# Kernel optimization log

Measured on AMD Instinct MI355X. Metric: run time of the kernel, lower is better.

The kernel has to match this reference:

```python
import jax, jax.numpy as jnp
import numpy as np

DEGREE = 7

def setup_inputs() -> dict:
    key = jax.random.key(0)
    k1, k2 = jax.random.split(key)
    input_dims, output_dims = 1024, 1024
    x = jax.random.normal(k1, (8192, input_dims), dtype=jnp.float32)
    std = 1.0 / (input_dims * (DEGREE + 1))
    lucas_coeffs = std * jax.random.normal(k2, (input_dims, output_dims, DEGREE + 1), dtype=jnp.float32)
    return {"x": x, "lucas_coeffs": lucas_coeffs}

def reference(x, lucas_coeffs):
    input_dims = lucas_coeffs.shape[0]
    x = x.reshape(-1, input_dims)
    x = jnp.tanh(x)
    # Lucas polynomial recurrence: L0=2, L1=x, L_i = x*L_{i-1} + L_{i-2}
    basis = [jnp.full_like(x, 2.0)]
    if DEGREE > 0:
        basis.append(x)
    for i in range(2, DEGREE + 1):
        basis.append(x * basis[-1] + basis[-2])
    lucas = jnp.stack(basis, axis=-1)  # [b, i, d]
    y = jnp.einsum('bid,iod->bo', lucas, lucas_coeffs)
    return y
```

## Files before the change

### kernel.cpp

```cpp
#include <hip/hip_runtime.h>
#include <hip/hip_bf16.h>


typedef __attribute__((ext_vector_type(8)))  short  short8;
typedef __attribute__((ext_vector_type(8)))  unsigned short ushort8;
typedef __attribute__((ext_vector_type(4)))  float  float4v;
typedef __attribute__((ext_vector_type(16))) float  float16v;
typedef __attribute__((ext_vector_type(4)))  unsigned int uint4v;

#define M_DIM 8192
#define I_DIM 1024
#define O_DIM 1024
#define K_DIM 8192
#define BM 256
#define BN 128
#define BK 64
#define KSPLIT 2
#define KHALF (K_DIM / KSPLIT)
#define NSTEP (KHALF / BK)

__device__ __forceinline__ unsigned short f2bf(float f) {
    unsigned int u = __float_as_uint(f);
    u += 0x7FFFu + ((u >> 16) & 1u);
    return (unsigned short)(u >> 16);
}

__global__ __launch_bounds__(256) void prep_kernel(const float* __restrict__ x,
                                                   const float* __restrict__ c,
                                                   unsigned short* __restrict__ T,
                                                   unsigned short* __restrict__ Bt,
                                                   float* __restrict__ outz) {
    int bid = blockIdx.x;
    const int zPart = (M_DIM * O_DIM) / (4 * 256);
    const int tPart = (M_DIM * I_DIM) / (8 * 256);
    if (bid < zPart) {
        int idx = (bid * 256 + threadIdx.x) * 4;
        const float4v z = {0.f, 0.f, 0.f, 0.f};
        *(float4v*)(outz + idx) = z;
    } else if (bid < zPart + tPart) {
        int idx = ((bid - zPart) * 256 + threadIdx.x) * 8;
        float4v v0 = *(const float4v*)(x + idx);
        float4v v1 = *(const float4v*)(x + idx + 4);
        unsigned short t[8];
        t[0] = f2bf(tanhf(v0[0])); t[1] = f2bf(tanhf(v0[1]));
        t[2] = f2bf(tanhf(v0[2])); t[3] = f2bf(tanhf(v0[3]));
        t[4] = f2bf(tanhf(v1[0])); t[5] = f2bf(tanhf(v1[1]));
        t[6] = f2bf(tanhf(v1[2])); t[7] = f2bf(tanhf(v1[3]));
        ushort8 o;
        #pragma unroll
        for (int p = 0; p < 4; ++p) { o[p] = t[2 * p]; o[4 + p] = t[2 * p + 1]; }
        *(ushort8*)(T + idx) = o;
    } else {
        int idx = (bid - zPart - tPart) * 256 + threadIdx.x;
        int i = idx >> 10;
        int o = idx & 1023;
        const float* src = c + (size_t)i * 8192 + o * 8;
        float4v lo = *(const float4v*)(src);
        float4v hi = *(const float4v*)(src + 4);
        ushort8 v;
        v[0] = f2bf(lo[0]); v[1] = f2bf(lo[1]); v[2] = f2bf(lo[2]); v[3] = f2bf(lo[3]);
        v[4] = f2bf(hi[0]); v[5] = f2bf(hi[1]); v[6] = f2bf(hi[2]); v[7] = f2bf(hi[3]);
        *(ushort8*)(Bt + (size_t)o * K_DIM + i * 8) = v;
    }
}

__device__ __forceinline__ short8 lucas_frag(unsigned int tb) {
    const float t = __uint_as_float(tb << 16);
    const float L2v = fmaf(t, t, 2.0f);
    const float L3v = fmaf(t, L2v, t);
    const float L4v = fmaf(t, L3v, L2v);
    const float L5v = fmaf(t, L4v, L3v);
    const float L6v = fmaf(t, L5v, L4v);
    const float L7v = fmaf(t, L6v, L5v);
    union { uint4v u; short8 s; } r;
#if __has_builtin(__builtin_amdgcn_cvt_pk_bf16_f32)
    {
        auto p0 = __builtin_amdgcn_cvt_pk_bf16_f32(2.0f, t);
        auto p1 = __builtin_amdgcn_cvt_pk_bf16_f32(L2v, L3v);
        auto p2 = __builtin_amdgcn_cvt_pk_bf16_f32(L4v, L5v);
        auto p3 = __builtin_amdgcn_cvt_pk_bf16_f32(L6v, L7v);
        __builtin_memcpy(&r.u[0], &p0, 4);
        __builtin_memcpy(&r.u[1], &p1, 4);
        __builtin_memcpy(&r.u[2], &p2, 4);
        __builtin_memcpy(&r.u[3], &p3, 4);
    }
#else
    {
        r.u[0] = 0x4000u | (tb << 16);
        r.u[1] = __builtin_amdgcn_perm(__float_as_uint(L3v), __float_as_uint(L2v), 0x07060302);
        r.u[2] = __builtin_amdgcn_perm(__float_as_uint(L5v), __float_as_uint(L4v), 0x07060302);
        r.u[3] = __builtin_amdgcn_perm(__float_as_uint(L7v), __float_as_uint(L6v), 0x07060302);
    }
#endif
    return r.s;
}

__global__ __launch_bounds__(256, 2) void gemm_kernel(const unsigned short* __restrict__ T,
                                                      const unsigned short* __restrict__ Bt,
                                                      float* __restrict__ out) {
    __shared__ unsigned short Bs[2][BN * BK];
    __shared__ unsigned short Ts[2][BM * 8];

    const int tid  = threadIdx.x;
    const int lane = tid & 63;
    const int wave = tid >> 6;
    const int n0 = blockIdx.x * BN;
    const int m0 = blockIdx.y * BM;
    const int k0 = blockIdx.z * KHALF;

    const int l32 = lane & 31;
    const int h   = lane >> 5;
    const int wml = wave * 64;

    const int srow   = lane >> 3;
    const int il     = lane & 7;
    const int gchunk = il ^ srow;

    float16v acc[2][4];
    #pragma unroll
    for (int a = 0; a < 2; ++a)
        #pragma unroll
        for (int b = 0; b < 4; ++b)
            #pragma unroll
            for (int e = 0; e < 16; ++e) acc[a][b][e] = 0.f;

    auto stage = [&](int buf, int kt) {
        #pragma unroll
        for (int r = 0; r < 4; ++r) {
            const int rowb = r * 32 + wave * 8;
            const unsigned short* gB = Bt + (size_t)(n0 + rowb + srow) * K_DIM + kt + gchunk * 8;
            __builtin_amdgcn_global_load_lds(
                (const __attribute__((address_space(1))) unsigned int*)gB,
                (__attribute__((address_space(3))) unsigned int*)&Bs[buf][rowb * BK], 16, 0, 0);
        }
        const unsigned short* gT = T + (size_t)(m0 + wml + lane) * I_DIM + kt / 8;
        __builtin_amdgcn_global_load_lds(
            (const __attribute__((address_space(1))) unsigned int*)gT,
            (__attribute__((address_space(3))) unsigned int*)&Ts[buf][wml * 8], 16, 0, 0);
    };

    stage(0, k0);
    __syncthreads();

    int cur = 0;
    for (int s = 0; s < NSTEP; ++s) {
        const int nxt = cur ^ 1;
        if (s + 1 < NSTEP) stage(nxt, k0 + (s + 1) * BK);

        unsigned long long tw[2];
        #pragma unroll
        for (int tt = 0; tt < 2; ++tt)
            tw[tt] = *(const unsigned long long*)&Ts[cur][(wml + tt * 32 + l32) * 8 + h * 4];

        #pragma unroll
        for (int kk = 0; kk < 4; ++kk) {
            short8 bfr[4];
            #pragma unroll
            for (int tn = 0; tn < 4; ++tn) {
                const int brow = tn * 32 + l32;
                bfr[tn] = *(const short8*)&Bs[cur][brow * BK + (((kk * 2 + h) ^ (brow & 7)) * 8)];
            }
            #pragma unroll
            for (int tt = 0; tt < 2; ++tt) {
                const short8 af = lucas_frag((unsigned int)((tw[tt] >> (16 * kk)) & 0xffffu));
                #pragma unroll
                for (int tn = 0; tn < 4; ++tn)
                    acc[tt][tn] = __builtin_amdgcn_mfma_f32_32x32x16_bf16(
                        af, bfr[tn], acc[tt][tn], 0, 0, 0);
            }
        }

        __syncthreads();
        cur = nxt;
    }

    #pragma unroll
    for (int tt = 0; tt < 2; ++tt) {
        #pragma unroll
        for (int tn = 0; tn < 4; ++tn) {
            const int col = n0 + tn * 32 + l32;
            #pragma unroll
            for (int reg = 0; reg < 16; ++reg) {
                const int row = m0 + wml + tt * 32 + (reg & 3) + 8 * (reg >> 2) + 4 * h;
                atomicAdd(&out[(size_t)row * O_DIM + col], acc[tt][tn][reg]);
            }
        }
    }
}

__global__ __launch_bounds__(256) void naive_kernel(const float* __restrict__ x,
                                                    const float* __restrict__ c,
                                                    float* __restrict__ out) {
    int idx = blockIdx.x * 256 + threadIdx.x;
    int b = idx >> 10;
    int o = idx & 1023;
    const float* xb = x + (size_t)b * I_DIM;
    float acc = 0.f;
    for (int i = 0; i < I_DIM; ++i) {
        float t = tanhf(xb[i]);
        float L[8];
        L[0] = 2.0f; L[1] = t;
        #pragma unroll
        for (int d = 2; d < 8; ++d) L[d] = t * L[d - 1] + L[d - 2];
        const float* cc = c + (size_t)i * 8192 + o * 8;
        #pragma unroll
        for (int d = 0; d < 8; ++d) acc += L[d] * cc[d];
    }
    out[idx] = acc;
}

extern "C" void kernel_launch(void* const* d_in, const int* in_sizes, int n_in,
                              void* d_out, int out_size, void* d_ws, size_t ws_size,
                              hipStream_t stream) {
    const float* x      = (const float*)d_in[0];
    const float* coeffs = (const float*)d_in[1];
    float* out = (float*)d_out;

    const size_t btBytes = (size_t)O_DIM * K_DIM * sizeof(unsigned short);
    const size_t tBytes  = (size_t)M_DIM * I_DIM * sizeof(unsigned short);

    if (ws_size >= btBytes + tBytes) {
        unsigned short* Bt = (unsigned short*)d_ws;
        unsigned short* T  = (unsigned short*)((char*)d_ws + btBytes);

        const int zBlocks = (M_DIM * O_DIM) / (4 * 256);
        const int tBlocks = (M_DIM * I_DIM) / (8 * 256);
        const int bBlocks = (I_DIM * O_DIM) / 256;
        prep_kernel<<<zBlocks + tBlocks + bBlocks, 256, 0, stream>>>(x, coeffs, T, Bt, out);

        dim3 grid(O_DIM / BN, M_DIM / BM, KSPLIT);
        gemm_kernel<<<grid, 256, 0, stream>>>(T, Bt, out);
    } else {
        naive_kernel<<<(M_DIM * O_DIM) / 256, 256, 0, stream>>>(x, coeffs, out);
    }
}
```

Baseline: 259.9 us.

## Shrink GEMM tile to 128x128 with 2x2 waves and LDS-transpose coefficient prep

The GEMM block tile is reduced from 256x128 to 128x128, with the four waves arranged 2x2 (64x64 each) instead of stacked along M. Accumulators per thread are halved and the occupancy hint is raised to 4 blocks per SM, giving twice as many blocks and more latency hiding. The trade is less B-tile reuse per block and more global traffic. Separately, the coefficient prep kernel now stages a 64x32 tile in shared memory, so both its reads of the fp32 coefficients and its writes of the transposed bf16 array are coalesced.

```diff
diff --git a/kernel.cpp b/kernel.cpp
--- a/kernel.cpp
+++ b/kernel.cpp
@@ -3,6 +3,7 @@
 
 
 typedef __attribute__((ext_vector_type(8)))  short  short8;
+typedef __attribute__((ext_vector_type(4)))  unsigned short ushort4v;
 typedef __attribute__((ext_vector_type(8)))  unsigned short ushort8;
 typedef __attribute__((ext_vector_type(4)))  float  float4v;
 typedef __attribute__((ext_vector_type(16))) float  float16v;
@@ -12,7 +13,7 @@
 #define I_DIM 1024
 #define O_DIM 1024
 #define K_DIM 8192
-#define BM 256
+#define BM 128
 #define BN 128
 #define BK 64
 #define KSPLIT 2
@@ -30,15 +31,16 @@
                                                    unsigned short* __restrict__ T,
                                                    unsigned short* __restrict__ Bt,
                                                    float* __restrict__ outz) {
-    int bid = blockIdx.x;
     const int zPart = (M_DIM * O_DIM) / (4 * 256);
     const int tPart = (M_DIM * I_DIM) / (8 * 256);
+    int bid = blockIdx.x;
+    int tid = threadIdx.x;
     if (bid < zPart) {
-        int idx = (bid * 256 + threadIdx.x) * 4;
+        int idx = (bid * 256 + tid) * 4;
         const float4v z = {0.f, 0.f, 0.f, 0.f};
         *(float4v*)(outz + idx) = z;
     } else if (bid < zPart + tPart) {
-        int idx = ((bid - zPart) * 256 + threadIdx.x) * 8;
+        int idx = ((bid - zPart) * 256 + tid) * 8;
         float4v v0 = *(const float4v*)(x + idx);
         float4v v1 = *(const float4v*)(x + idx + 4);
         unsigned short t[8];
@@ -51,16 +53,28 @@
         for (int p = 0; p < 4; ++p) { o[p] = t[2 * p]; o[4 + p] = t[2 * p + 1]; }
         *(ushort8*)(T + idx) = o;
     } else {
-        int idx = (bid - zPart - tPart) * 256 + threadIdx.x;
-        int i = idx >> 10;
-        int o = idx & 1023;
-        const float* src = c + (size_t)i * 8192 + o * 8;
-        float4v lo = *(const float4v*)(src);
-        float4v hi = *(const float4v*)(src + 4);
-        ushort8 v;
-        v[0] = f2bf(lo[0]); v[1] = f2bf(lo[1]); v[2] = f2bf(lo[2]); v[3] = f2bf(lo[3]);
-        v[4] = f2bf(hi[0]); v[5] = f2bf(hi[1]); v[6] = f2bf(hi[2]); v[7] = f2bf(hi[3]);
-        *(ushort8*)(Bt + (size_t)o * K_DIM + i * 8) = v;
+        __shared__ unsigned short S[32][64 * 8 + 8];
+        int tb = bid - zPart - tPart;
+        const int i0 = (tb >> 5) * 64;
+        const int o0 = (tb & 31) * 32;
+        #pragma unroll 4
+        for (int p = 0; p < 16; ++p) {
+            const int il = p * 4 + (tid >> 6);
+            const int e  = (tid & 63) * 4;
+            const float* src = c + (size_t)(i0 + il) * 8192 + o0 * 8 + e;
+            float4v v = *(const float4v*)src;
+            ushort4v u;
+            u[0] = f2bf(v[0]); u[1] = f2bf(v[1]); u[2] = f2bf(v[2]); u[3] = f2bf(v[3]);
+            *(ushort4v*)&S[e >> 3][il * 8 + (e & 7)] = u;
+        }
+        __syncthreads();
+        #pragma unroll 4
+        for (int q = 0; q < 16; ++q) {
+            const int ol = q * 2 + (tid >> 7);
+            const int ch = (tid & 127) * 4;
+            ushort4v u = *(const ushort4v*)&S[ol][ch];
+            *(ushort4v*)(Bt + (size_t)(o0 + ol) * K_DIM + i0 * 8 + ch) = u;
+        }
     }
 }
 
@@ -95,7 +109,7 @@
     return r.s;
 }
 
-__global__ __launch_bounds__(256, 2) void gemm_kernel(const unsigned short* __restrict__ T,
+__global__ __launch_bounds__(256, 4) void gemm_kernel(const unsigned short* __restrict__ T,
                                                       const unsigned short* __restrict__ Bt,
                                                       float* __restrict__ out) {
     __shared__ unsigned short Bs[2][BN * BK];
@@ -108,19 +122,20 @@
     const int m0 = blockIdx.y * BM;
     const int k0 = blockIdx.z * KHALF;
 
+    const int wm0 = (wave >> 1) * 64;
+    const int wn0 = (wave & 1) * 64;
     const int l32 = lane & 31;
     const int h   = lane >> 5;
-    const int wml = wave * 64;
 
     const int srow   = lane >> 3;
     const int il     = lane & 7;
     const int gchunk = il ^ srow;
 
-    float16v acc[2][4];
+    float16v acc[2][2];
     #pragma unroll
     for (int a = 0; a < 2; ++a)
         #pragma unroll
-        for (int b = 0; b < 4; ++b)
+        for (int b = 0; b < 2; ++b)
             #pragma unroll
             for (int e = 0; e < 16; ++e) acc[a][b][e] = 0.f;
 
@@ -133,10 +148,12 @@
                 (const __attribute__((address_space(1))) unsigned int*)gB,
                 (__attribute__((address_space(3))) unsigned int*)&Bs[buf][rowb * BK], 16, 0, 0);
         }
-        const unsigned short* gT = T + (size_t)(m0 + wml + lane) * I_DIM + kt / 8;
-        __builtin_amdgcn_global_load_lds(
-            (const __attribute__((address_space(1))) unsigned int*)gT,
-            (__attribute__((address_space(3))) unsigned int*)&Ts[buf][wml * 8], 16, 0, 0);
+        if (wave < 2) {
+            const unsigned short* gT = T + (size_t)(m0 + wave * 64 + lane) * I_DIM + kt / 8;
+            __builtin_amdgcn_global_load_lds(
+                (const __attribute__((address_space(1))) unsigned int*)gT,
+                (__attribute__((address_space(3))) unsigned int*)&Ts[buf][wave * 64 * 8], 16, 0, 0);
+        }
     };
 
     stage(0, k0);
@@ -150,21 +167,21 @@
         unsigned long long tw[2];
         #pragma unroll
         for (int tt = 0; tt < 2; ++tt)
-            tw[tt] = *(const unsigned long long*)&Ts[cur][(wml + tt * 32 + l32) * 8 + h * 4];
+            tw[tt] = *(const unsigned long long*)&Ts[cur][(wm0 + tt * 32 + l32) * 8 + h * 4];
 
         #pragma unroll
         for (int kk = 0; kk < 4; ++kk) {
-            short8 bfr[4];
-            #pragma unroll
-            for (int tn = 0; tn < 4; ++tn) {
-                const int brow = tn * 32 + l32;
+            short8 bfr[2];
+            #pragma unroll
+            for (int tn = 0; tn < 2; ++tn) {
+                const int brow = wn0 + tn * 32 + l32;
                 bfr[tn] = *(const short8*)&Bs[cur][brow * BK + (((kk * 2 + h) ^ (brow & 7)) * 8)];
             }
             #pragma unroll
             for (int tt = 0; tt < 2; ++tt) {
                 const short8 af = lucas_frag((unsigned int)((tw[tt] >> (16 * kk)) & 0xffffu));
                 #pragma unroll
-                for (int tn = 0; tn < 4; ++tn)
+                for (int tn = 0; tn < 2; ++tn)
                     acc[tt][tn] = __builtin_amdgcn_mfma_f32_32x32x16_bf16(
                         af, bfr[tn], acc[tt][tn], 0, 0, 0);
             }
@@ -177,11 +194,11 @@
     #pragma unroll
     for (int tt = 0; tt < 2; ++tt) {
         #pragma unroll
-        for (int tn = 0; tn < 4; ++tn) {
-            const int col = n0 + tn * 32 + l32;
+        for (int tn = 0; tn < 2; ++tn) {
+            const int col = n0 + wn0 + tn * 32 + l32;
             #pragma unroll
             for (int reg = 0; reg < 16; ++reg) {
-                const int row = m0 + wml + tt * 32 + (reg & 3) + 8 * (reg >> 2) + 4 * h;
+                const int row = m0 + wm0 + tt * 32 + (reg & 3) + 8 * (reg >> 2) + 4 * h;
                 atomicAdd(&out[(size_t)row * O_DIM + col], acc[tt][tn][reg]);
             }
         }
@@ -225,8 +242,8 @@
 
         const int zBlocks = (M_DIM * O_DIM) / (4 * 256);
         const int tBlocks = (M_DIM * I_DIM) / (8 * 256);
-        const int bBlocks = (I_DIM * O_DIM) / 256;
-        prep_kernel<<<zBlocks + tBlocks + bBlocks, 256, 0, stream>>>(x, coeffs, T, Bt, out);
+        const int xBlocks = (I_DIM / 64) * (I_DIM / 32);
+        prep_kernel<<<zBlocks + tBlocks + xBlocks, 256, 0, stream>>>(x, coeffs, T, Bt, out);
 
         dim3 grid(O_DIM / BN, M_DIM / BM, KSPLIT);
         gemm_kernel<<<grid, 256, 0, stream>>>(T, Bt, out);
```

Result: no change. 259.3 us (-0.2%).
